# Kernel tuning notes

Measured on AMD Instinct MI355X. Metric: run time of the kernel, lower is better.

## Reference

```python
import jax, jax.numpy as jnp
import numpy as np
import math

H = 512
NH = 8
HD = H // NH


def _lin_params(key, out_dim, in_dim):
    k1, k2 = jax.random.split(key)
    bound = 1.0 / math.sqrt(in_dim)
    w = jax.random.uniform(k1, (out_dim, in_dim), minval=-bound, maxval=bound, dtype=jnp.float32)
    b = jax.random.uniform(k2, (out_dim,), minval=-bound, maxval=bound, dtype=jnp.float32)
    return w, b


def setup_inputs() -> dict:
    key = jax.random.key(0)
    ks = jax.random.split(key, 16)
    B, L = 8, 1024
    inp = {
        'hidden_states': jax.random.normal(ks[0], (B, L, H), dtype=jnp.float32),
        'text': jax.random.normal(ks[1], (B, L, H), dtype=jnp.float32),
    }
    names = ['q_img', 'k_img', 'v_img', 'q_txt', 'k_txt', 'v_txt', 'out_img', 'out_txt']
    for i, n in enumerate(names):
        w, b = _lin_params(ks[2 + i], H, H)
        inp['w_' + n] = w
        inp['b_' + n] = b
    wcat, bcat = _lin_params(ks[10], H, 2 * H)
    inp['w_cat'] = wcat
    inp['b_cat'] = bcat
    # nn.MultiheadAttention params: in_proj [3H, H], out_proj [H, H]
    inp['in_proj_w'] = jax.random.normal(ks[11], (3 * H, H), dtype=jnp.float32) * (1.0 / math.sqrt(H))
    inp['in_proj_b'] = jnp.zeros((3 * H,), dtype=jnp.float32)
    pw, pb = _lin_params(ks[12], H, H)
    inp['out_proj_w'] = pw
    inp['out_proj_b'] = pb
    return inp


def _lin(x, w, b):
    return x @ w.T + b


def _heads(x):
    B, L, _ = x.shape
    return x.reshape(B, L, NH, HD).transpose(0, 2, 1, 3)  # [B, NH, L, HD]


def _attn(q, k, v):
    # q,k,v: [B, NH, L, HD]; dropout is identity in eval mode
    scores = jnp.einsum('bhqd,bhkd->bhqk', q, k) / math.sqrt(HD)
    probs = jax.nn.softmax(scores, axis=-1)
    ctx = jnp.einsum('bhqk,bhkd->bhqd', probs, v)
    B, _, L, _ = ctx.shape
    return ctx.transpose(0, 2, 1, 3).reshape(B, L, H)


def reference(hidden_states, text,
              w_q_img, b_q_img, w_k_img, b_k_img, w_v_img, b_v_img,
              w_q_txt, b_q_txt, w_k_txt, b_k_txt, w_v_txt, b_v_txt,
              w_out_img, b_out_img, w_out_txt, b_out_txt,
              w_cat, b_cat, in_proj_w, in_proj_b, out_proj_w, out_proj_b):
    q_img = _heads(_lin(hidden_states, w_q_img, b_q_img))
    k_img = _heads(_lin(hidden_states, w_k_img, b_k_img))
    v_img = _heads(_lin(hidden_states, w_v_img, b_v_img))
    q_txt = _heads(_lin(text, w_q_txt, b_q_txt))
    k_txt = _heads(_lin(text, w_k_txt, b_k_txt))
    v_txt = _heads(_lin(text, w_v_txt, b_v_txt))

    ctx_img = _attn(q_img, k_img, v_img)
    ctx_txt = _attn(q_txt, k_txt, v_txt)
    ctx_it = _attn(q_img, k_txt, v_txt)
    ctx_ti = _attn(q_txt, k_img, v_img)

    out_img = _lin((ctx_img + ctx_it) * 0.5, w_out_img, b_out_img)
    out_txt = _lin((ctx_txt + ctx_ti) * 0.5, w_out_txt, b_out_txt)
    out = _lin(jnp.concatenate([out_img, out_txt], axis=2), w_cat, b_cat)

    # attention pooling (nn.MultiheadAttention self-attention, batch-major math)
    qkv = _lin(out, in_proj_w, in_proj_b)
    q, k, v = jnp.split(qkv, 3, axis=-1)
    ctx = _attn(_heads(q), _heads(k), _heads(v))
    return _lin(ctx, out_proj_w, out_proj_b)
```

## Files before the change

### kernel.cpp

```cpp
#include <hip/hip_runtime.h>

typedef unsigned short u16;
typedef __attribute__((ext_vector_type(4))) unsigned short u16x4;
typedef __attribute__((ext_vector_type(8))) unsigned short u16x8;
typedef __attribute__((ext_vector_type(4))) float f32x4;
typedef __attribute__((ext_vector_type(8))) __bf16 bf16x8;
typedef __attribute__((ext_vector_type(2))) unsigned int u32x2;
typedef __attribute__((ext_vector_type(4))) unsigned int u32x4;

#define WS_XH    0UL
#define WS_XT    8388608UL
#define WS_W     16777216UL
#define WS_BQI   24117248UL
#define WS_BQT   24123392UL
#define WS_QKVI  24129536UL
#define WS_QKVT  49295360UL
#define WS_VTI   74461184UL
#define WS_VTT   82849792UL
#define WS_CTXIA 91238400UL
#define WS_CTXTA 99627008UL
#define WS_OCAT  108015616UL
#define WS_OUT2  24129536UL
#define WS_QKVP  32518144UL
#define WS_VTP   57683968UL
#define WS_CTXP  66072576UL

#define SCALE_LOG2E_O8 0.18033688011112042f


__device__ __forceinline__ u16 f2bf(float f) {
  unsigned u = __float_as_uint(f);
  u += 0x7fffu + ((u >> 16) & 1u);
  return (u16)(u >> 16);
}
__device__ __forceinline__ float bf2f(u16 v) {
  return __uint_as_float(((unsigned)v) << 16);
}
__device__ __forceinline__ bf16x8 as_bf(u16x8 v) { return __builtin_bit_cast(bf16x8, v); }
__device__ __forceinline__ f32x4 mfma16(bf16x8 a, bf16x8 b, f32x4 c) {
  return __builtin_amdgcn_mfma_f32_16x16x32_bf16(a, b, c, 0, 0, 0);
}
__device__ __forceinline__ unsigned cvt_pk_bf16(float lo, float hi) {
  unsigned r;
  asm("v_cvt_pk_bf16_f32 %0, %1, %2" : "=v"(r) : "v"(lo), "v"(hi));
  return r;
}

__global__ __launch_bounds__(256) void cvt_f32_bf16(const float* __restrict__ s0,
                                                    const float* __restrict__ s1,
                                                    u16* __restrict__ d0,
                                                    u16* __restrict__ d1, int n) {
  const float* s = blockIdx.y ? s1 : s0;
  u16* d = blockIdx.y ? d1 : d0;
  int i = (blockIdx.x * 256 + threadIdx.x) * 4;
  if (i >= n) return;
  float4 v = *(const float4*)(s + i);
  u16x4 o;
  o[0] = f2bf(v.x); o[1] = f2bf(v.y); o[2] = f2bf(v.z); o[3] = f2bf(v.w);
  *(u16x4*)(d + i) = o;
}

__global__ __launch_bounds__(256) void prep_weights(
    const float* __restrict__ wqi, const float* __restrict__ wki, const float* __restrict__ wvi,
    const float* __restrict__ wqt, const float* __restrict__ wkt, const float* __restrict__ wvt,
    const float* __restrict__ woi, const float* __restrict__ wot,
    const float* __restrict__ wc,  const float* __restrict__ wip, const float* __restrict__ wop,
    const float* __restrict__ bqi, const float* __restrict__ bki, const float* __restrict__ bvi,
    const float* __restrict__ bqt, const float* __restrict__ bkt, const float* __restrict__ bvt,
    u16* __restrict__ wdst, float* __restrict__ bi, float* __restrict__ bt) {
  int i = blockIdx.x * 256 + threadIdx.x;
  if (i < 786432) {
    const float* s = i < 262144 ? wqi : (i < 524288 ? wki : wvi);
    wdst[i] = f2bf(s[i & 262143]);
  } else if (i < 1572864) {
    int j = i - 786432;
    const float* s = j < 262144 ? wqt : (j < 524288 ? wkt : wvt);
    wdst[i] = f2bf(s[j & 262143]);
  } else if (i < 1835008) wdst[i] = f2bf(woi[i - 1572864]);
  else if (i < 2097152)   wdst[i] = f2bf(wot[i - 1835008]);
  else if (i < 2621440)   wdst[i] = f2bf(wc [i - 2097152]);
  else if (i < 3407872)   wdst[i] = f2bf(wip[i - 2621440]);
  else if (i < 3670016)   wdst[i] = f2bf(wop[i - 3407872]);
  else if (i < 3671552) {
    int j = i - 3670016;
    bi[j] = j < 512 ? bqi[j] : (j < 1024 ? bki[j - 512] : bvi[j - 1024]);
  } else if (i < 3673088) {
    int j = i - 3671552;
    bt[j] = j < 512 ? bqt[j] : (j < 1024 ? bkt[j - 512] : bvt[j - 1024]);
  }
}

__global__ __launch_bounds__(256) void gemm_bf16(
    const u16* __restrict__ A, const u16* __restrict__ A2, int lda,
    const u16* __restrict__ W,
    const float* __restrict__ bias, u16* __restrict__ C, int ldc, int coff, int K,
    int f32out, int qcols, float qscale, u16* __restrict__ vtout,
    long zdA, long zdA2, long zdW, long zdB, long zdC, long zdVT, int zdCoff) {
  if (blockIdx.z) {
    A += zdA;
    if (A2) A2 += zdA2;
    W += zdW; bias += zdB; C += zdC;
    if (vtout) vtout += zdVT;
    coff += zdCoff;
  }
  __shared__ __align__(16) u16 As[2][8 * 512];
  __shared__ __align__(16) u16 Bs[2][8 * 512];
  const int tid = threadIdx.x, lane = tid & 63, wv = tid >> 6;
  const int wm = wv >> 1, wn = wv & 1;
  const int ln15 = lane & 15;
  const int m0 = blockIdx.x * 128, n0 = blockIdx.y * 128;

  const int srow = lane & 15, skc = lane >> 4;
  const u16* gA0 = A + (long)(m0 + wv * 32 + srow) * lda + skc * 8;
  const u16* gA1 = gA0 + (long)16 * lda;
  const u16* gW0 = W + (long)(n0 + wv * 32 + srow) * K + skc * 8;
  const u16* gW1 = gW0 + (long)16 * K;
  const u16* gA20 = A2 + (long)(m0 + wv * 32 + srow) * lda + skc * 8;
  const u16* gA21 = gA20 + (long)16 * lda;

  f32x4 acc[4][4];
#pragma unroll
  for (int j = 0; j < 4; ++j) {
    float bv = bias[n0 + wn * 64 + j * 16 + ln15];
#pragma unroll
    for (int i = 0; i < 4; ++i) acc[i][j] = f32x4{bv, bv, bv, bv};
  }

  u16x8 ra0 = *(const u16x8*)(gA0);
  u16x8 ra1 = *(const u16x8*)(gA1);
  u16x8 rb0 = *(const u16x8*)(gW0);
  u16x8 rb1 = *(const u16x8*)(gW1);
  u16x8 rc0, rc1;
  if (A2) { rc0 = *(const u16x8*)(gA20); rc1 = *(const u16x8*)(gA21); }

  int buf = 0;
  for (int k0 = 0; k0 < K; k0 += 32, buf ^= 1) {
    u16x8 wa0 = ra0, wa1 = ra1;
    if (A2) {
#pragma unroll
      for (int u = 0; u < 8; ++u) {
        wa0[u] = f2bf(bf2f(ra0[u]) + bf2f(rc0[u]));
        wa1[u] = f2bf(bf2f(ra1[u]) + bf2f(rc1[u]));
      }
    }
    u16* la = As[buf] + (wv * 2) * 512;
    u16* lb = Bs[buf] + (wv * 2) * 512;
    *(u16x8*)(la + lane * 8) = wa0;
    *(u16x8*)(la + 512 + lane * 8) = wa1;
    *(u16x8*)(lb + lane * 8) = rb0;
    *(u16x8*)(lb + 512 + lane * 8) = rb1;
    __syncthreads();
    if (k0 + 32 < K) {
      ra0 = *(const u16x8*)(gA0 + k0 + 32);
      ra1 = *(const u16x8*)(gA1 + k0 + 32);
      rb0 = *(const u16x8*)(gW0 + k0 + 32);
      rb1 = *(const u16x8*)(gW1 + k0 + 32);
      if (A2) { rc0 = *(const u16x8*)(gA20 + k0 + 32); rc1 = *(const u16x8*)(gA21 + k0 + 32); }
    }

    bf16x8 af[4], bfr[4];
#pragma unroll
    for (int i = 0; i < 4; ++i)
      af[i] = as_bf(*(const u16x8*)(As[buf] + (wm * 4 + i) * 512 + lane * 8));
#pragma unroll
    for (int j = 0; j < 4; ++j)
      bfr[j] = as_bf(*(const u16x8*)(Bs[buf] + (wn * 4 + j) * 512 + lane * 8));
#pragma unroll
    for (int i = 0; i < 4; ++i)
#pragma unroll
      for (int j = 0; j < 4; ++j) acc[i][j] = mfma16(af[i], bfr[j], acc[i][j]);
  }
  const int quad = lane >> 4;
  const int qr4 = quad * 4;
  if (vtout && n0 >= 1024) {
#pragma unroll
    for (int j = 0; j < 4; ++j) {
      int col = n0 + wn * 64 + j * 16 + ln15;
      int dg = col - 1024;
#pragma unroll
      for (int i = 0; i < 4; ++i) {
        int row0 = m0 + wm * 64 + i * 16 + qr4;
        long vr = ((long)(row0 >> 10) * 8 + (dg >> 6)) * 64 + (dg & 63);
        u16x4 ov;
#pragma unroll
        for (int r = 0; r < 4; ++r) ov[r] = f2bf(acc[i][j][r]);
        *(u16x4*)(vtout + vr * 1024 + (row0 & 1023)) = ov;
      }
    }
    return;
  }
  float colsc[4];
#pragma unroll
  for (int j = 0; j < 4; ++j)
    colsc[j] = (n0 + wn * 64 + j * 16 < qcols) ? qscale : 1.0f;
#pragma unroll
  for (int i = 0; i < 4; ++i)
#pragma unroll
    for (int r = 0; r < 4; ++r) {
      int row = m0 + wm * 64 + i * 16 + qr4 + r;
      long cidx = (long)row * ldc + coff + n0 + wn * 64 + ln15;
      if (f32out) {
        float* cf = (float*)C + cidx;
#pragma unroll
        for (int j = 0; j < 4; ++j) cf[j * 16] = acc[i][j][r] * colsc[j];
      } else {
        u16* cp = C + cidx;
#pragma unroll
        for (int j = 0; j < 4; ++j) cp[j * 16] = f2bf(acc[i][j][r] * colsc[j]);
      }
    }
}

template <int NQF, bool DUAL>
__global__ __launch_bounds__(256) void attn_flash(
    const u16* __restrict__ Q0, const u16* __restrict__ Q1, int ldq,
    const u16* __restrict__ K0, const u16* __restrict__ VT0,
    const u16* __restrict__ K1, const u16* __restrict__ VT1, int ldk,
    u16* __restrict__ O00, u16* __restrict__ O01,
    u16* __restrict__ O10, u16* __restrict__ O11, int ldo, float outscale) {
  __shared__ __align__(16) u16 Kt[2][32][72];
  __shared__ __align__(16) u16 Vt[2][64][40];
  const int tid = threadIdx.x, lane = tid & 63, wv = tid >> 6;
  const int ln15 = lane & 15, quad = lane >> 4, q8 = quad * 8;
  const int h = blockIdx.y;

  const u16 *Q, *K, *VT;
  u16* O;
  int qtile, b;
  if constexpr (DUAL) {
    qtile = blockIdx.x >> 1;
    const int phase = blockIdx.x & 1;
    const int qsel = blockIdx.z & 1;
    b = blockIdx.z >> 1;
    Q = qsel ? Q1 : Q0;
    const int ksel = qsel ^ phase;
    K = ksel ? K1 : K0;
    VT = ksel ? VT1 : VT0;
    O = qsel ? (phase ? O11 : O10) : (phase ? O01 : O00);
  } else {
    qtile = blockIdx.x;
    b = blockIdx.z;
    Q = Q0; K = K0; VT = VT0; O = O00;
  }
  const long qrow = (long)b * 1024 + qtile * (NQF * 64) + wv * (NQF * 16);

  bf16x8 qf[NQF][2];
#pragma unroll
  for (int qi = 0; qi < NQF; ++qi) {
    const u16* qp = Q + (qrow + qi * 16 + ln15) * ldq + h * 64;
    qf[qi][0] = as_bf(*(const u16x8*)(qp + q8));
    qf[qi][1] = as_bf(*(const u16x8*)(qp + 32 + q8));
  }

  u16x8 ones_u;
#pragma unroll
  for (int j = 0; j < 8; ++j) ones_u[j] = 0x3F80;
  const bf16x8 onesb = as_bf(ones_u);

  const int kk = tid >> 3, dc = (tid & 7) * 8;
  const int vd = tid >> 2;
  const int ko = (tid & 3) * 8;
  const int vs0 = ((tid & 1) << 4) | ((tid & 2) << 1);
  const u16* Kbase = K + ((long)b * 1024 + kk) * ldk + h * 64 + dc;
  const u16* Vbase = VT + ((long)((b * 8 + h) * 64 + vd)) * 1024 + ko;

  f32x4 o[NQF][4];
  f32x4 lacc[NQF];
#pragma unroll
  for (int qi = 0; qi < NQF; ++qi) {
    lacc[qi] = f32x4{0.f, 0.f, 0.f, 0.f};
#pragma unroll
    for (int j = 0; j < 4; ++j) o[qi][j] = f32x4{0.f, 0.f, 0.f, 0.f};
  }

  u32x4 kreg = *(const u32x4*)(Kbase);
  u32x4 vreg = *(const u32x4*)(Vbase);

  int cur = 0;
  for (int k0 = 0; k0 < 1024; k0 += 32, cur ^= 1) {
    *(u32x4*)(&Kt[cur][kk][dc]) = kreg;
    u32x2 vlo = {vreg[0], vreg[1]}, vhi = {vreg[2], vreg[3]};
    *(u32x2*)(&Vt[cur][vd][vs0]) = vlo;
    *(u32x2*)(&Vt[cur][vd][vs0 + 8]) = vhi;
    __syncthreads();
    if (k0 + 32 < 1024) {
      kreg = *(const u32x4*)(Kbase + (long)(k0 + 32) * ldk);
      vreg = *(const u32x4*)(Vbase + (k0 + 32));
    }

    f32x4 st[2][NQF];
    __builtin_amdgcn_s_setprio(1);
#pragma unroll
    for (int kt = 0; kt < 2; ++kt) {
      bf16x8 ka0 = as_bf(*(const u16x8*)(&Kt[cur][kt * 16 + ln15][q8]));
      bf16x8 ka1 = as_bf(*(const u16x8*)(&Kt[cur][kt * 16 + ln15][32 + q8]));
#pragma unroll
      for (int qi = 0; qi < NQF; ++qi) {
        f32x4 z = f32x4{0.f, 0.f, 0.f, 0.f};
        z = mfma16(ka0, qf[qi][0], z);
        z = mfma16(ka1, qf[qi][1], z);
        st[kt][qi] = z;
      }
    }
    __builtin_amdgcn_s_setprio(0);

    bf16x8 pb[NQF];
#pragma unroll
    for (int qi = 0; qi < NQF; ++qi) {
      float p00 = __builtin_amdgcn_exp2f(st[0][qi][0]);
      float p01 = __builtin_amdgcn_exp2f(st[0][qi][1]);
      float p02 = __builtin_amdgcn_exp2f(st[0][qi][2]);
      float p03 = __builtin_amdgcn_exp2f(st[0][qi][3]);
      float p10 = __builtin_amdgcn_exp2f(st[1][qi][0]);
      float p11 = __builtin_amdgcn_exp2f(st[1][qi][1]);
      float p12 = __builtin_amdgcn_exp2f(st[1][qi][2]);
      float p13 = __builtin_amdgcn_exp2f(st[1][qi][3]);
      u32x4 pk;
      pk[0] = cvt_pk_bf16(p00, p01);
      pk[1] = cvt_pk_bf16(p02, p03);
      pk[2] = cvt_pk_bf16(p10, p11);
      pk[3] = cvt_pk_bf16(p12, p13);
      pb[qi] = as_bf(__builtin_bit_cast(u16x8, pk));
      lacc[qi] = mfma16(onesb, pb[qi], lacc[qi]);
    }
    __builtin_amdgcn_s_setprio(1);
#pragma unroll
    for (int j = 0; j < 4; ++j) {
      bf16x8 av = as_bf(*(const u16x8*)(&Vt[cur][j * 16 + ln15][q8]));
#pragma unroll
      for (int qi = 0; qi < NQF; ++qi) o[qi][j] = mfma16(av, pb[qi], o[qi][j]);
    }
    __builtin_amdgcn_s_setprio(0);
  }

#pragma unroll
  for (int qi = 0; qi < NQF; ++qi) {
    float inv = outscale / lacc[qi][0];
    long row = qrow + qi * 16 + ln15;
#pragma unroll
    for (int j = 0; j < 4; ++j) {
      u16x4 ov;
#pragma unroll
      for (int r = 0; r < 4; ++r) ov[r] = f2bf(o[qi][j][r] * inv);
      *(u16x4*)(O + row * ldo + h * 64 + j * 16 + quad * 4) = ov;
    }
  }
}

extern "C" void kernel_launch(void* const* d_in, const int* in_sizes, int n_in,
                              void* d_out, int out_size, void* d_ws, size_t ws_size,
                              hipStream_t stream) {
  const float* hidden = (const float*)d_in[0];
  const float* text   = (const float*)d_in[1];
  const float* wqi = (const float*)d_in[2];  const float* bqi = (const float*)d_in[3];
  const float* wki = (const float*)d_in[4];  const float* bki = (const float*)d_in[5];
  const float* wvi = (const float*)d_in[6];  const float* bvi = (const float*)d_in[7];
  const float* wqt = (const float*)d_in[8];  const float* bqt = (const float*)d_in[9];
  const float* wkt = (const float*)d_in[10]; const float* bkt = (const float*)d_in[11];
  const float* wvt = (const float*)d_in[12]; const float* bvt = (const float*)d_in[13];
  const float* woi = (const float*)d_in[14]; const float* boi = (const float*)d_in[15];
  const float* wot = (const float*)d_in[16]; const float* bot = (const float*)d_in[17];
  const float* wc  = (const float*)d_in[18]; const float* bc  = (const float*)d_in[19];
  const float* wip = (const float*)d_in[20]; const float* bip = (const float*)d_in[21];
  const float* wop = (const float*)d_in[22]; const float* bop = (const float*)d_in[23];

  char* ws = (char*)d_ws;
  u16* XH    = (u16*)(ws + WS_XH);
  u16* XT    = (u16*)(ws + WS_XT);
  u16* WB    = (u16*)(ws + WS_W);
  float* BQI = (float*)(ws + WS_BQI);
  float* BQT = (float*)(ws + WS_BQT);
  u16* QKVI  = (u16*)(ws + WS_QKVI);
  u16* QKVT  = (u16*)(ws + WS_QKVT);
  u16* VTI   = (u16*)(ws + WS_VTI);
  u16* VTT   = (u16*)(ws + WS_VTT);
  u16* CTXIA = (u16*)(ws + WS_CTXIA);
  u16* CTXIB = (u16*)(ws + WS_XH);
  u16* CTXTA = (u16*)(ws + WS_CTXTA);
  u16* CTXTB = (u16*)(ws + WS_XT);
  u16* OCAT  = (u16*)(ws + WS_OCAT);
  u16* OUT2  = (u16*)(ws + WS_OUT2);
  u16* QKVP  = (u16*)(ws + WS_QKVP);
  u16* VTP   = (u16*)(ws + WS_VTP);
  u16* CTXP  = (u16*)(ws + WS_CTXP);

  u16* WQKVI = WB;
  u16* WOUTI = WB + 1572864;
  u16* WCAT  = WB + 2097152;
  u16* WINP  = WB + 2621440;
  u16* WOUTP = WB + 3407872;

  const int NACT = 8192 * 512;

  cvt_f32_bf16<<<dim3(NACT / 1024, 2), 256, 0, stream>>>(hidden, text, XH, XT, NACT);
  prep_weights<<<dim3(14348), 256, 0, stream>>>(wqi, wki, wvi, wqt, wkt, wvt, woi, wot,
                                                wc, wip, wop, bqi, bki, bvi, bqt, bkt, bvt,
                                                WB, BQI, BQT);
  gemm_bf16<<<dim3(64, 12, 2), 256, 0, stream>>>(
      XH, nullptr, 512, WQKVI, BQI, QKVI, 1536, 0, 512, 0, 512, SCALE_LOG2E_O8, VTI,
      4194304, 0, 786432, 1536, 12582912, 4194304, 0);
  attn_flash<2, true><<<dim3(16, 8, 16), 256, 0, stream>>>(
      QKVI, QKVT, 1536, QKVI + 512, VTI, QKVT + 512, VTT, 1536,
      CTXIA, CTXIB, CTXTA, CTXTB, 512, 0.5f);
  gemm_bf16<<<dim3(64, 4, 2), 256, 0, stream>>>(
      CTXIA, CTXIB, 512, WOUTI, boi, OCAT, 1024, 0, 512, 0, 0, 1.0f, nullptr,
      4194304, 4194304, 262144, (long)(bot - boi),
      0, 0, 512);
  gemm_bf16<<<dim3(64, 4, 1), 256, 0, stream>>>(
      OCAT, nullptr, 1024, WCAT, bc, OUT2, 512, 0, 1024, 0, 0, 1.0f, nullptr,
      0, 0, 0, 0, 0, 0, 0);
  gemm_bf16<<<dim3(64, 12, 1), 256, 0, stream>>>(
      OUT2, nullptr, 512, WINP, bip, QKVP, 1536, 0, 512, 0, 512, SCALE_LOG2E_O8, VTP,
      0, 0, 0, 0, 0, 0, 0);
  attn_flash<2, false><<<dim3(8, 8, 8), 256, 0, stream>>>(
      QKVP, nullptr, 1536, QKVP + 512, VTP, nullptr, nullptr, 1536,
      CTXP, nullptr, nullptr, nullptr, 512, 1.0f);
  gemm_bf16<<<dim3(64, 4, 1), 256, 0, stream>>>(
      CTXP, nullptr, 512, WOUTP, bop, (u16*)d_out, 512, 0, 512, 1, 0, 1.0f, nullptr,
      0, 0, 0, 0, 0, 0, 0);
}
```

Baseline: 381.4 us.

## Replace LDS-staged GEMM with per-wave register-direct 64x64 tile GEMM

Result: slower. 502.6 us (+31.8%).

```diff
diff --git a/kernel.cpp b/kernel.cpp
--- a/kernel.cpp
+++ b/kernel.cpp
@@ -90,96 +90,71 @@
   }
 }
 
-__global__ __launch_bounds__(256) void gemm_bf16(
+template <bool A2ADD>
+__global__ __launch_bounds__(256) void gemm_reg(
     const u16* __restrict__ A, const u16* __restrict__ A2, int lda,
     const u16* __restrict__ W,
     const float* __restrict__ bias, u16* __restrict__ C, int ldc, int coff, int K,
-    int f32out, int qcols, float qscale, u16* __restrict__ vtout,
+    int f32out, int qcols, float qscale, u16* __restrict__ vtout, int ntn,
     long zdA, long zdA2, long zdW, long zdB, long zdC, long zdVT, int zdCoff) {
   if (blockIdx.z) {
     A += zdA;
-    if (A2) A2 += zdA2;
+    if (A2ADD) A2 += zdA2;
     W += zdW; bias += zdB; C += zdC;
     if (vtout) vtout += zdVT;
     coff += zdCoff;
   }
-  __shared__ __align__(16) u16 As[2][8 * 512];
-  __shared__ __align__(16) u16 Bs[2][8 * 512];
   const int tid = threadIdx.x, lane = tid & 63, wv = tid >> 6;
-  const int wm = wv >> 1, wn = wv & 1;
-  const int ln15 = lane & 15;
-  const int m0 = blockIdx.x * 128, n0 = blockIdx.y * 128;
-
-  const int srow = lane & 15, skc = lane >> 4;
-  const u16* gA0 = A + (long)(m0 + wv * 32 + srow) * lda + skc * 8;
-  const u16* gA1 = gA0 + (long)16 * lda;
-  const u16* gW0 = W + (long)(n0 + wv * 32 + srow) * K + skc * 8;
-  const u16* gW1 = gW0 + (long)16 * K;
-  const u16* gA20 = A2 + (long)(m0 + wv * 32 + srow) * lda + skc * 8;
-  const u16* gA21 = gA20 + (long)16 * lda;
+  const int tile = blockIdx.x * 4 + wv;
+  const int mt = tile / ntn, nt = tile - mt * ntn;
+  const int m0 = mt * 64, n0 = nt * 64;
+  const int ln15 = lane & 15, quad = lane >> 4, q8 = quad * 8;
+
+  const u16* pa  = A + (long)(m0 + ln15) * lda + q8;
+  const u16* pw  = W + (long)(n0 + ln15) * K + q8;
+  const u16* pa2 = A2ADD ? (A2 + (long)(m0 + ln15) * lda + q8) : nullptr;
+  const long la16 = (long)16 * lda;
+  const long lw16 = (long)16 * K;
 
   f32x4 acc[4][4];
 #pragma unroll
   for (int j = 0; j < 4; ++j) {
-    float bv = bias[n0 + wn * 64 + j * 16 + ln15];
+    float bv = bias[n0 + j * 16 + ln15];
 #pragma unroll
     for (int i = 0; i < 4; ++i) acc[i][j] = f32x4{bv, bv, bv, bv};
   }
 
-  u16x8 ra0 = *(const u16x8*)(gA0);
-  u16x8 ra1 = *(const u16x8*)(gA1);
-  u16x8 rb0 = *(const u16x8*)(gW0);
-  u16x8 rb1 = *(const u16x8*)(gW1);
-  u16x8 rc0, rc1;
-  if (A2) { rc0 = *(const u16x8*)(gA20); rc1 = *(const u16x8*)(gA21); }
-
-  int buf = 0;
-  for (int k0 = 0; k0 < K; k0 += 32, buf ^= 1) {
-    u16x8 wa0 = ra0, wa1 = ra1;
-    if (A2) {
-#pragma unroll
-      for (int u = 0; u < 8; ++u) {
-        wa0[u] = f2bf(bf2f(ra0[u]) + bf2f(rc0[u]));
-        wa1[u] = f2bf(bf2f(ra1[u]) + bf2f(rc1[u]));
+#pragma unroll 2
+  for (int k0 = 0; k0 < K; k0 += 32) {
+    bf16x8 af[4], bfr[4];
+#pragma unroll
+    for (int i = 0; i < 4; ++i) {
+      u16x8 v = *(const u16x8*)(pa + (long)i * la16 + k0);
+      if constexpr (A2ADD) {
+        u16x8 v2 = *(const u16x8*)(pa2 + (long)i * la16 + k0);
+#pragma unroll
+        for (int u = 0; u < 8; ++u) v[u] = f2bf(bf2f(v[u]) + bf2f(v2[u]));
       }
-    }
-    u16* la = As[buf] + (wv * 2) * 512;
-    u16* lb = Bs[buf] + (wv * 2) * 512;
-    *(u16x8*)(la + lane * 8) = wa0;
-    *(u16x8*)(la + 512 + lane * 8) = wa1;
-    *(u16x8*)(lb + lane * 8) = rb0;
-    *(u16x8*)(lb + 512 + lane * 8) = rb1;
-    __syncthreads();
-    if (k0 + 32 < K) {
-      ra0 = *(const u16x8*)(gA0 + k0 + 32);
-      ra1 = *(const u16x8*)(gA1 + k0 + 32);
-      rb0 = *(const u16x8*)(gW0 + k0 + 32);
-      rb1 = *(const u16x8*)(gW1 + k0 + 32);
-      if (A2) { rc0 = *(const u16x8*)(gA20 + k0 + 32); rc1 = *(const u16x8*)(gA21 + k0 + 32); }
-    }
-
-    bf16x8 af[4], bfr[4];
+      af[i] = as_bf(v);
+    }
+#pragma unroll
+    for (int j = 0; j < 4; ++j)
+      bfr[j] = as_bf(*(const u16x8*)(pw + (long)j * lw16 + k0));
 #pragma unroll
     for (int i = 0; i < 4; ++i)
-      af[i] = as_bf(*(const u16x8*)(As[buf] + (wm * 4 + i) * 512 + lane * 8));
-#pragma unroll
-    for (int j = 0; j < 4; ++j)
-      bfr[j] = as_bf(*(const u16x8*)(Bs[buf] + (wn * 4 + j) * 512 + lane * 8));
-#pragma unroll
-    for (int i = 0; i < 4; ++i)
 #pragma unroll
       for (int j = 0; j < 4; ++j) acc[i][j] = mfma16(af[i], bfr[j], acc[i][j]);
   }
-  const int quad = lane >> 4;
+
   const int qr4 = quad * 4;
   if (vtout && n0 >= 1024) {
 #pragma unroll
     for (int j = 0; j < 4; ++j) {
-      int col = n0 + wn * 64 + j * 16 + ln15;
+      int col = n0 + j * 16 + ln15;
       int dg = col - 1024;
 #pragma unroll
       for (int i = 0; i < 4; ++i) {
-        int row0 = m0 + wm * 64 + i * 16 + qr4;
+        int row0 = m0 + i * 16 + qr4;
         long vr = ((long)(row0 >> 10) * 8 + (dg >> 6)) * 64 + (dg & 63);
         u16x4 ov;
 #pragma unroll
@@ -192,13 +167,13 @@
   float colsc[4];
 #pragma unroll
   for (int j = 0; j < 4; ++j)
-    colsc[j] = (n0 + wn * 64 + j * 16 < qcols) ? qscale : 1.0f;
+    colsc[j] = (n0 + j * 16 < qcols) ? qscale : 1.0f;
 #pragma unroll
   for (int i = 0; i < 4; ++i)
 #pragma unroll
     for (int r = 0; r < 4; ++r) {
-      int row = m0 + wm * 64 + i * 16 + qr4 + r;
-      long cidx = (long)row * ldc + coff + n0 + wn * 64 + ln15;
+      int row = m0 + i * 16 + qr4 + r;
+      long cidx = (long)row * ldc + coff + n0 + ln15;
       if (f32out) {
         float* cf = (float*)C + cidx;
 #pragma unroll
@@ -396,26 +371,26 @@
   prep_weights<<<dim3(14348), 256, 0, stream>>>(wqi, wki, wvi, wqt, wkt, wvt, woi, wot,
                                                 wc, wip, wop, bqi, bki, bvi, bqt, bkt, bvt,
                                                 WB, BQI, BQT);
-  gemm_bf16<<<dim3(64, 12, 2), 256, 0, stream>>>(
-      XH, nullptr, 512, WQKVI, BQI, QKVI, 1536, 0, 512, 0, 512, SCALE_LOG2E_O8, VTI,
+  gemm_reg<false><<<dim3(768, 1, 2), 256, 0, stream>>>(
+      XH, nullptr, 512, WQKVI, BQI, QKVI, 1536, 0, 512, 0, 512, SCALE_LOG2E_O8, VTI, 24,
       4194304, 0, 786432, 1536, 12582912, 4194304, 0);
   attn_flash<2, true><<<dim3(16, 8, 16), 256, 0, stream>>>(
       QKVI, QKVT, 1536, QKVI + 512, VTI, QKVT + 512, VTT, 1536,
       CTXIA, CTXIB, CTXTA, CTXTB, 512, 0.5f);
-  gemm_bf16<<<dim3(64, 4, 2), 256, 0, stream>>>(
-      CTXIA, CTXIB, 512, WOUTI, boi, OCAT, 1024, 0, 512, 0, 0, 1.0f, nullptr,
+  gemm_reg<true><<<dim3(256, 1, 2), 256, 0, stream>>>(
+      CTXIA, CTXIB, 512, WOUTI, boi, OCAT, 1024, 0, 512, 0, 0, 1.0f, nullptr, 8,
       4194304, 4194304, 262144, (long)(bot - boi),
       0, 0, 512);
-  gemm_bf16<<<dim3(64, 4, 1), 256, 0, stream>>>(
-      OCAT, nullptr, 1024, WCAT, bc, OUT2, 512, 0, 1024, 0, 0, 1.0f, nullptr,
+  gemm_reg<false><<<dim3(256, 1, 1), 256, 0, stream>>>(
+      OCAT, nullptr, 1024, WCAT, bc, OUT2, 512, 0, 1024, 0, 0, 1.0f, nullptr, 8,
       0, 0, 0, 0, 0, 0, 0);
-  gemm_bf16<<<dim3(64, 12, 1), 256, 0, stream>>>(
-      OUT2, nullptr, 512, WINP, bip, QKVP, 1536, 0, 512, 0, 512, SCALE_LOG2E_O8, VTP,
+  gemm_reg<false><<<dim3(768, 1, 1), 256, 0, stream>>>(
+      OUT2, nullptr, 512, WINP, bip, QKVP, 1536, 0, 512, 0, 512, SCALE_LOG2E_O8, VTP, 24,
       0, 0, 0, 0, 0, 0, 0);
   attn_flash<2, false><<<dim3(8, 8, 8), 256, 0, stream>>>(
       QKVP, nullptr, 1536, QKVP + 512, VTP, nullptr, nullptr, 1536,
       CTXP, nullptr, nullptr, nullptr, 512, 1.0f);
-  gemm_bf16<<<dim3(64, 4, 1), 256, 0, stream>>>(
-      CTXP, nullptr, 512, WOUTP, bop, (u16*)d_out, 512, 0, 512, 1, 0, 1.0f, nullptr,
+  gemm_reg<false><<<dim3(256, 1, 1), 256, 0, stream>>>(
+      CTXP, nullptr, 512, WOUTP, bop, (u16*)d_out, 512, 0, 512, 1, 0, 1.0f, nullptr, 8,
       0, 0, 0, 0, 0, 0, 0);
 }
```
